# Kernel optimization log

Measured on AMD Instinct MI355X. Metric: run time of the kernel, lower is better.

Reference implementation:

```python
import jax, jax.numpy as jnp
import numpy as np

CROP = 7
OFFSET = 0.5
MIN_LEVEL, MAX_LEVEL = 2, 5


def _crop_level(feat, boxes, level):
    """Crop-and-resize all boxes at one pyramid level (TF model-garden math).

    feat:  [B, H, W, C] level feature map
    boxes: [B, N, 4] un-normalized [y1, x1, y2, x2] in image coords
    returns [B, N, CROP, CROP, C]
    """
    B, H, W, C = feat.shape
    scale = jnp.asarray(2.0 ** level, feat.dtype)
    b = boxes / scale  # map to level coordinates
    y1, x1, y2, x2 = b[..., 0], b[..., 1], b[..., 2], b[..., 3]
    # sample grid centers: y1 + (i + offset) * h / crop_size
    t = (jnp.arange(CROP, dtype=feat.dtype) + OFFSET) / CROP  # [CROP]
    gy = y1[..., None] + t * (y2 - y1)[..., None]  # [B, N, CROP]
    gx = x1[..., None] + t * (x2 - x1)[..., None]  # [B, N, CROP]
    # floor, clamp low at 0 (matches _compute_grid_positions)
    y0 = jnp.maximum(jnp.floor(gy), 0.0)
    x0 = jnp.maximum(jnp.floor(gx), 0.0)
    ly, lx = gy - y0, gx - x0
    ky = jnp.stack([1.0 - ly, ly], axis=-1)  # [B, N, CROP, 2]
    kx = jnp.stack([1.0 - lx, lx], axis=-1)  # [B, N, CROP, 2]
    # integer gather indices, clamped to feature boundary
    yi = jnp.stack([jnp.minimum(y0, H - 1.0), jnp.minimum(y0 + 1.0, H - 1.0)], -1).astype(jnp.int32)  # [B,N,CROP,2]
    xi = jnp.stack([jnp.minimum(x0, W - 1.0), jnp.minimum(x0 + 1.0, W - 1.0)], -1).astype(jnp.int32)
    # flat spatial index [B, N, I, 2, J, 2]
    flat = yi[:, :, :, :, None, None] * W + xi[:, :, None, None, :, :]
    featf = feat.reshape(B, H * W, C)
    gath = jax.vmap(lambda f, idx: jnp.take(f, idx, axis=0))(featf, flat)  # [B,N,I,2,J,2,C]
    # bilinear combine: sum over the 2x2 corner axes with kernel weights
    return jnp.einsum('bnipjqc,bnip,bnjq->bnijc', gath, ky, kx)


def setup_inputs() -> dict:
    key = jax.random.key(0)
    ks = jax.random.split(key, 6)
    B, N, C = 2, 512, 256
    out = {}
    for li, lvl in enumerate(range(MIN_LEVEL, MAX_LEVEL + 1)):
        s = 1024 // (2 ** lvl)
        out[f'feats_l{lvl}'] = jax.random.normal(ks[li], (B, s, s, C), jnp.float32)
    yx = jax.random.uniform(ks[4], (B, N, 2), jnp.float32, 0.0, 800.0)
    hw = jax.random.uniform(ks[5], (B, N, 2), jnp.float32, 16.0, 224.0)
    out['boxes'] = jnp.concatenate([yx, yx + hw], axis=-1)  # [y1,x1,y2,x2]
    return out


def reference(feats_l2, feats_l3, feats_l4, feats_l5, boxes):
    feats = {2: feats_l2, 3: feats_l3, 4: feats_l4, 5: feats_l5}
    # AFP path: crop every box at every level (specified_level loop)
    outs = [_crop_level(feats[l], boxes, l) for l in range(MIN_LEVEL, MAX_LEVEL + 1)]
    return jnp.stack(outs, axis=0)  # [n_levels, B, N, CROP, CROP, C]
```

## Files before the change

### kernel.cpp

```cpp
#include <hip/hip_runtime.h>

#define CROP   7
#define NBOX   512
#define BATCH  2
#define NLVL   4
#define CH     256
#define C4     (CH / 4)


__global__ __launch_bounds__(256) void roi_align_kernel(
    const float* __restrict__ f2, const float* __restrict__ f3,
    const float* __restrict__ f4, const float* __restrict__ f5,
    const float* __restrict__ boxes, float4* __restrict__ out)
{
#pragma clang fp contract(off)
    const unsigned tid  = blockIdx.x * blockDim.x + threadIdx.x;
    const unsigned c4   = tid & (C4 - 1);
    const unsigned cell = tid >> 6;

    const unsigned j = cell % CROP;
    unsigned t = cell / CROP;
    const unsigned i = t % CROP;
    t /= CROP;
    const unsigned n = t % NBOX;
    t /= NBOX;
    const unsigned b = t % BATCH;
    const unsigned l = t / BATCH;

    const float* feat;
    unsigned H;
    if      (l == 0) { feat = f2; H = 256; }
    else if (l == 1) { feat = f3; H = 128; }
    else if (l == 2) { feat = f4; H = 64;  }
    else             { feat = f5; H = 32;  }
    const float inv_scale = 1.0f / (float)(4u << l);

    const float* bx = boxes + (((size_t)b * NBOX + n) << 2);
    const float y1 = bx[0] * inv_scale;
    const float x1 = bx[1] * inv_scale;
    const float y2 = bx[2] * inv_scale;
    const float x2 = bx[3] * inv_scale;

    const float ti = ((float)i + 0.5f) / 7.0f;
    const float tj = ((float)j + 0.5f) / 7.0f;
    const float gy = y1 + ti * (y2 - y1);
    const float gx = x1 + tj * (x2 - x1);

    const float y0 = fmaxf(floorf(gy), 0.0f);
    const float x0 = fmaxf(floorf(gx), 0.0f);
    const float ly = gy - y0;
    const float lx = gx - x0;

    const float Hm1 = (float)(H - 1);
    const int yi0 = (int)fminf(y0,        Hm1);
    const int yi1 = (int)fminf(y0 + 1.0f, Hm1);
    const int xi0 = (int)fminf(x0,        Hm1);
    const int xi1 = (int)fminf(x0 + 1.0f, Hm1);

    const float w00 = (1.0f - ly) * (1.0f - lx);
    const float w01 = (1.0f - ly) * lx;
    const float w10 = ly * (1.0f - lx);
    const float w11 = ly * lx;

    const float4* fp = (const float4*)feat;
    const size_t rowb = (size_t)b * H * H * C4;
    const float4 v00 = fp[rowb + ((size_t)yi0 * H + xi0) * C4 + c4];
    const float4 v01 = fp[rowb + ((size_t)yi0 * H + xi1) * C4 + c4];
    const float4 v10 = fp[rowb + ((size_t)yi1 * H + xi0) * C4 + c4];
    const float4 v11 = fp[rowb + ((size_t)yi1 * H + xi1) * C4 + c4];

    float4 r;
    r.x = w00 * v00.x + w01 * v01.x + w10 * v10.x + w11 * v11.x;
    r.y = w00 * v00.y + w01 * v01.y + w10 * v10.y + w11 * v11.y;
    r.z = w00 * v00.z + w01 * v01.z + w10 * v10.z + w11 * v11.z;
    r.w = w00 * v00.w + w01 * v01.w + w10 * v10.w + w11 * v11.w;

    out[tid] = r;
}

extern "C" void kernel_launch(void* const* d_in, const int* in_sizes, int n_in,
                              void* d_out, int out_size, void* d_ws, size_t ws_size,
                              hipStream_t stream) {
    const float* f2    = (const float*)d_in[0];
    const float* f3    = (const float*)d_in[1];
    const float* f4    = (const float*)d_in[2];
    const float* f5    = (const float*)d_in[3];
    const float* boxes = (const float*)d_in[4];
    float4* out = (float4*)d_out;

    const unsigned total_threads = NLVL * BATCH * NBOX * CROP * CROP * C4;
    const unsigned block = 256;
    const unsigned grid  = total_threads / block;

    roi_align_kernel<<<grid, block, 0, stream>>>(f2, f3, f4, f5, boxes, out);
}
```

Measured before the change: 342.3 us.

## Remap grid to one block per box row with XCD-aware swizzle and nontemporal stores

Each block now handles one crop row (7 cells x 64 lanes) of a single box, and the block index is swizzled so that consecutive blocks on the same XCD (g & 7) handle the same box's rows. This is meant to improve L2 reuse of the feature rows gathered for a box and to remove the div/mod index decoding per thread. Output writes use nontemporal stores to avoid polluting the cache with the large streaming output. Block size grows to 448, which may change occupancy.

New measurement: 332.9 us. 2.7% less time.

```diff
diff --git a/kernel.cpp b/kernel.cpp
--- a/kernel.cpp
+++ b/kernel.cpp
@@ -7,25 +7,27 @@
 #define CH     256
 #define C4     (CH / 4)
 
+typedef float nfloat4 __attribute__((ext_vector_type(4)));
 
-__global__ __launch_bounds__(256) void roi_align_kernel(
+
+__global__ __launch_bounds__(448) void roi_align_kernel(
     const float* __restrict__ f2, const float* __restrict__ f3,
     const float* __restrict__ f4, const float* __restrict__ f5,
-    const float* __restrict__ boxes, float4* __restrict__ out)
+    const float* __restrict__ boxes, nfloat4* __restrict__ out)
 {
 #pragma clang fp contract(off)
-    const unsigned tid  = blockIdx.x * blockDim.x + threadIdx.x;
-    const unsigned c4   = tid & (C4 - 1);
-    const unsigned cell = tid >> 6;
+    const unsigned lane = threadIdx.x & 63;
+    const unsigned j    = threadIdx.x >> 6;
 
-    const unsigned j = cell % CROP;
-    unsigned t = cell / CROP;
-    const unsigned i = t % CROP;
-    t /= CROP;
-    const unsigned n = t % NBOX;
-    t /= NBOX;
-    const unsigned b = t % BATCH;
-    const unsigned l = t / BATCH;
+    const unsigned g   = blockIdx.x;
+    const unsigned xcd = g & 7;
+    const unsigned rem = g >> 3;
+    const unsigned q8  = rem / 7;
+    const unsigned i   = rem - q8 * 7;
+    const unsigned q   = (q8 << 3) | xcd;
+    const unsigned n   = q & (NBOX - 1);
+    const unsigned b   = (q >> 9) & (BATCH - 1);
+    const unsigned l   = q >> 10;
 
     const float* feat;
     unsigned H;
@@ -62,20 +64,21 @@
     const float w10 = ly * (1.0f - lx);
     const float w11 = ly * lx;
 
-    const float4* fp = (const float4*)feat;
+    const nfloat4* fp = (const nfloat4*)feat;
     const size_t rowb = (size_t)b * H * H * C4;
-    const float4 v00 = fp[rowb + ((size_t)yi0 * H + xi0) * C4 + c4];
-    const float4 v01 = fp[rowb + ((size_t)yi0 * H + xi1) * C4 + c4];
-    const float4 v10 = fp[rowb + ((size_t)yi1 * H + xi0) * C4 + c4];
-    const float4 v11 = fp[rowb + ((size_t)yi1 * H + xi1) * C4 + c4];
+    const nfloat4 v00 = fp[rowb + ((size_t)yi0 * H + xi0) * C4 + lane];
+    const nfloat4 v01 = fp[rowb + ((size_t)yi0 * H + xi1) * C4 + lane];
+    const nfloat4 v10 = fp[rowb + ((size_t)yi1 * H + xi0) * C4 + lane];
+    const nfloat4 v11 = fp[rowb + ((size_t)yi1 * H + xi1) * C4 + lane];
 
-    float4 r;
+    nfloat4 r;
     r.x = w00 * v00.x + w01 * v01.x + w10 * v10.x + w11 * v11.x;
     r.y = w00 * v00.y + w01 * v01.y + w10 * v10.y + w11 * v11.y;
     r.z = w00 * v00.z + w01 * v01.z + w10 * v10.z + w11 * v11.z;
     r.w = w00 * v00.w + w01 * v01.w + w10 * v10.w + w11 * v11.w;
 
-    out[tid] = r;
+    const size_t oidx = (((size_t)q * (CROP * CROP) + i * CROP + j) << 6) + lane;
+    __builtin_nontemporal_store(r, &out[oidx]);
 }
 
 extern "C" void kernel_launch(void* const* d_in, const int* in_sizes, int n_in,
@@ -86,11 +89,10 @@
     const float* f4    = (const float*)d_in[2];
     const float* f5    = (const float*)d_in[3];
     const float* boxes = (const float*)d_in[4];
-    float4* out = (float4*)d_out;
+    nfloat4* out = (nfloat4*)d_out;
 
-    const unsigned total_threads = NLVL * BATCH * NBOX * CROP * CROP * C4;
-    const unsigned block = 256;
-    const unsigned grid  = total_threads / block;
+    const unsigned grid  = NLVL * BATCH * NBOX * CROP;
+    const unsigned block = CROP * 64;
 
     roi_align_kernel<<<grid, block, 0, stream>>>(f2, f3, f4, f5, boxes, out);
 }
```
